# Optimization experiments

Measured on AMD Instinct MI355X. Metric: run time of the kernel, lower is better.

The kernel has to match this reference:

```python
import jax, jax.numpy as jnp
import numpy as np

B, L, D, H, K = 8, 2048, 1024, 4, 4
HD = D // H  # head_dim = 256
EPS_NORM = 1e-12  # F.normalize clamp
RMS_EPS = 1e-05


def setup_inputs() -> dict:
    key = jax.random.key(0)
    ks = jax.random.split(key, 10)
    s = 0.02
    return {
        "x": jax.random.normal(ks[0], (B, L, D), dtype=jnp.float32),
        "Wq": jax.random.normal(ks[1], (D, D), dtype=jnp.float32) * s,
        "Wk": jax.random.normal(ks[2], (D, D), dtype=jnp.float32) * s,
        "Wv": jax.random.normal(ks[3], (D, D), dtype=jnp.float32) * s,
        "cq": jax.random.normal(ks[4], (D, 1, K), dtype=jnp.float32) * 0.2,
        "ck": jax.random.normal(ks[5], (D, 1, K), dtype=jnp.float32) * 0.2,
        "cv": jax.random.normal(ks[6], (D, 1, K), dtype=jnp.float32) * 0.2,
        "Wbeta": jax.random.normal(ks[7], (H, D), dtype=jnp.float32) * s,
        "rms_w": jnp.ones((D,), dtype=jnp.float32),
        "Wout": jax.random.normal(ks[8], (D, D), dtype=jnp.float32) * s,
    }


def _causal_dwconv_silu(y, w):
    # y: [B, L, D], w: [D, 1, K] (torch Conv1d depthwise weight, cross-correlation)
    yt = jnp.transpose(y, (0, 2, 1))  # [B, D, L]
    out = jax.lax.conv_general_dilated(
        yt, w, window_strides=(1,), padding=[(K - 1, 0)],
        dimension_numbers=("NCH", "OIH", "NCH"), feature_group_count=D)
    return jnp.transpose(jax.nn.silu(out), (0, 2, 1))  # [B, L, D]


def _l2norm(x):
    n = jnp.sqrt(jnp.sum(x * x, axis=-1, keepdims=True))
    return x / jnp.maximum(n, EPS_NORM)


def reference(x, Wq, Wk, Wv, cq, ck, cv, Wbeta, rms_w, Wout):
    q = x @ Wq.T
    k = x @ Wk.T
    v = x @ Wv.T
    # depthwise causal conv + silu, then reshape to heads, then silu again (as in source)
    q = jax.nn.silu(_causal_dwconv_silu(q, cq).reshape(B, L, H, HD))
    k = jax.nn.silu(_causal_dwconv_silu(k, ck).reshape(B, L, H, HD))
    v = jax.nn.silu(_causal_dwconv_silu(v, cv).reshape(B, L, H, HD))
    q = _l2norm(q)
    k = _l2norm(k)
    beta = jax.nn.sigmoid(x @ Wbeta.T)  # [B, L, H]

    # time-major for scan: [L, B, H, d]
    kT = jnp.transpose(k, (1, 0, 2, 3))
    qT = jnp.transpose(q, (1, 0, 2, 3))
    vT = jnp.transpose(v, (1, 0, 2, 3))
    bT = jnp.transpose(beta, (1, 0, 2))  # [L, B, H]

    S0 = jnp.zeros((B, H, HD, HD), dtype=x.dtype)

    def step(S, inp):
        k_t, q_t, v_t, b_t = inp
        Sk = jnp.einsum("bhij,bhj->bhi", S, k_t)
        upd = (Sk - v_t)[..., :, None] * k_t[..., None, :]  # outer product [B,H,d,d]
        S = S - b_t[..., None, None] * upd
        o = jnp.einsum("bhij,bhj->bhi", S, q_t)
        return S, o

    S_final, o_all = jax.lax.scan(step, S0, (kT, qT, vT, bT))
    o = o_all[-1].reshape(B, D)  # only last timestep's output is used

    # RMSNorm + output projection
    o = o * jax.lax.rsqrt(jnp.mean(o * o, axis=-1, keepdims=True) + RMS_EPS) * rms_w
    o = o @ Wout.T
    return o, S_final
```

## Files before the change

### kernel.cpp

```cpp
#include <hip/hip_runtime.h>

#define LL 2048
#define BB 8
#define DD 1024
#define HH 4
#define HD 256

#define AS1 __attribute__((address_space(1)))
#define AS3 __attribute__((address_space(3)))

typedef __attribute__((ext_vector_type(8))) short short8;
typedef __attribute__((ext_vector_type(4))) float f32x4;
typedef unsigned short u16;
typedef unsigned int u32;

static __device__ __forceinline__ u16 f2bf(float f) {
    u32 u = __float_as_uint(f);
    return (u16)((u + 0x7fffu + ((u >> 16) & 1u)) >> 16);
}
static __device__ __forceinline__ float bf2f(u16 v) {
    return __uint_as_float(((u32)v) << 16);
}
static __device__ __forceinline__ float silu_f(float x) { return x / (1.0f + __expf(-x)); }
static __device__ __forceinline__ float silu2_fast(float x) {
    float s1 = x * __builtin_amdgcn_rcpf(1.0f + __expf(-x));
    return s1 * __builtin_amdgcn_rcpf(1.0f + __expf(-s1));
}

#define BAR_LGKM() do { \
    asm volatile("s_waitcnt lgkmcnt(0)" ::: "memory"); \
    __builtin_amdgcn_s_barrier(); \
    __builtin_amdgcn_sched_barrier(0); \
} while (0)

static __device__ __forceinline__ void cvt8_body(const float* __restrict__ in,
                                                 u16* __restrict__ out, int blk, int n) {
    int i = (blk * 256 + (int)threadIdx.x) * 8;
    if (i >= n) return;
    float4 a = *(const float4*)(in + i);
    float4 b = *(const float4*)(in + i + 4);
    uint4 pk;
    pk.x = (u32)f2bf(a.x) | ((u32)f2bf(a.y) << 16);
    pk.y = (u32)f2bf(a.z) | ((u32)f2bf(a.w) << 16);
    pk.z = (u32)f2bf(b.x) | ((u32)f2bf(b.y) << 16);
    pk.w = (u32)f2bf(b.z) | ((u32)f2bf(b.w) << 16);
    *(uint4*)(out + i) = pk;
}

__global__ __launch_bounds__(256) void front_kernel(
    const float* __restrict__ x, const float* __restrict__ Wk, const float* __restrict__ Wv,
    const float* __restrict__ Wbeta, const float* __restrict__ Wq,
    u16* __restrict__ XB, u16* __restrict__ WKVB, float* __restrict__ BETA,
    u16* __restrict__ RQ)
{
    const int blk = blockIdx.x;
    const int tid = threadIdx.x;
    if (blk < 8192) {
        cvt8_body(x, XB, blk, 16777216);
    } else if (blk < 8704) {
        cvt8_body(Wk, WKVB, blk - 8192, 1048576);
    } else if (blk < 9216) {
        cvt8_body(Wv, WKVB + 1048576, blk - 8704, 1048576);
    } else if (blk < 13312) {
        const int row = (blk - 9216) * 4 + (tid >> 6);
        const int lane = tid & 63;
        const float* xr = x + (long)row * DD + lane * 16;
        float4 xv[4];
#pragma unroll
        for (int u = 0; u < 4; u++) xv[u] = *(const float4*)(xr + u * 4);
#pragma unroll
        for (int h = 0; h < 4; h++) {
            const float* wr = Wbeta + (long)h * DD + lane * 16;
            float s = 0.f;
#pragma unroll
            for (int u = 0; u < 4; u++) {
                float4 w = *(const float4*)(wr + u * 4);
                s += xv[u].x * w.x + xv[u].y * w.y + xv[u].z * w.z + xv[u].w * w.w;
            }
#pragma unroll
            for (int m = 1; m < 64; m <<= 1) s += __shfl_xor(s, m);
            if (lane == 0) BETA[(long)row * HH + h] = 1.0f / (1.0f + __expf(-s));
        }
    } else {
        const int gid = (blk - 13312) * 4 + (tid >> 6);
        const int lane = tid & 63;
        const int m = gid >> 10;
        const int n = gid & 1023;
        const int b = m >> 2, j = m & 3;
        const int l = LL - 4 + j;
        const float* xr = x + ((long)b * LL + l) * DD + lane * 16;
        const float* wr = Wq + (long)n * DD + lane * 16;
        float s = 0.f;
#pragma unroll
        for (int u = 0; u < 4; u++) {
            float4 a = *(const float4*)(xr + u * 4);
            float4 w = *(const float4*)(wr + u * 4);
            s += a.x * w.x + a.y * w.y + a.z * w.z + a.w * w.w;
        }
#pragma unroll
        for (int mm = 1; mm < 64; mm <<= 1) s += __shfl_xor(s, mm);
        if (lane == 0) RQ[(long)m * DD + n] = f2bf(s);
    }
}

__global__ __launch_bounds__(256, 2) void gemm_bf16(const u16* __restrict__ A,
                                                    const u16* __restrict__ W,
                                                    u16* __restrict__ C, int ldc) {
    __shared__ __align__(16) u16 sm[32768];
    const int tid = threadIdx.x;
    const int w = tid >> 6, lane = tid & 63, g = lane >> 4, c = lane & 15;
    const int m0 = blockIdx.y * 128, n0 = blockIdx.x * 128;
    const int wm = (w >> 1) * 64, wn = (w & 1) * 64;

    f32x4 acc[4][4];
#pragma unroll
    for (int i = 0; i < 4; i++)
#pragma unroll
        for (int j = 0; j < 4; j++) acc[i][j] = (f32x4){0.f, 0.f, 0.f, 0.f};

    const int sr = tid >> 3;
    const int cb = (tid & 7) * 16;

#define GLDSG(gp, lofs) __builtin_amdgcn_global_load_lds((const AS1 void*)(gp), \
        (AS3 void*)((AS3 char*)(char*)sm + (lofs)), 16, 0, 0)

#define GSTAGE(kt, bi)                                                        \
    {                                                                         \
        const char* ab = (const char*)(A + (long)m0 * DD + (kt) * 64);        \
        const char* wb = (const char*)(W + (long)n0 * DD + (kt) * 64);        \
        _Pragma("unroll")                                                     \
        for (int i = 0; i < 4; i++) {                                         \
            int r = i * 32 + sr;                                              \
            int so = r * 2048 + (cb ^ ((r & 7) << 4));                        \
            int dof = (bi) * 32768 + i * 4096 + tid * 16;                     \
            GLDSG(ab + so, dof);                                              \
            GLDSG(wb + so, dof + 16384);                                      \
        }                                                                     \
    }

    GSTAGE(0, 0);
    __syncthreads();

    const int sw = (c & 7) << 4;
    for (int kt = 0; kt < 16; kt++) {
        const int bi = kt & 1;
        if (kt < 15) GSTAGE(kt + 1, bi ^ 1);
        const int ba = bi * 32768;
#pragma unroll
        for (int ks = 0; ks < 2; ks++) {
            short8 av[4], bvv[4];
#pragma unroll
            for (int mt = 0; mt < 4; mt++)
                av[mt] = *(const short8*)((const char*)sm + ba +
                         (wm + 16 * mt + c) * 128 + ((ks * 64 + g * 16) ^ sw));
#pragma unroll
            for (int nt = 0; nt < 4; nt++)
                bvv[nt] = *(const short8*)((const char*)sm + ba + 16384 +
                          (wn + 16 * nt + c) * 128 + ((ks * 64 + g * 16) ^ sw));
#pragma unroll
            for (int mt = 0; mt < 4; mt++)
#pragma unroll
                for (int nt = 0; nt < 4; nt++)
                    acc[mt][nt] = __builtin_amdgcn_mfma_f32_16x16x32_bf16(av[mt], bvv[nt], acc[mt][nt], 0, 0, 0);
        }
        __syncthreads();
    }

#pragma unroll
    for (int mt = 0; mt < 4; mt++)
#pragma unroll
        for (int nt = 0; nt < 4; nt++)
#pragma unroll
            for (int r = 0; r < 4; r++)
                C[(long)(m0 + wm + 16 * mt + 4 * g + r) * ldc + n0 + wn + 16 * nt + c] =
                    f2bf(acc[mt][nt][r]);
#undef GSTAGE
#undef GLDSG
}

__global__ __launch_bounds__(256, 2) void prep_fused(
    const u16* __restrict__ R, const float* __restrict__ ck, const float* __restrict__ cv,
    const float* __restrict__ cq, const u16* __restrict__ RQ, const float* __restrict__ BETA,
    u16* __restrict__ LK_g, u16* __restrict__ BKT_g, u16* __restrict__ LV_g,
    u16* __restrict__ QN)
{
    __shared__ __align__(16) char pm[66560];
    const int blk = blockIdx.x;
    const int tid = threadIdx.x;

    if (blk >= 1024) {
        const int b = blk - 1024;
        const int d = tid * 4;
        float w0[4], w1[4], w2[4], w3[4];
        const float4* cw4 = (const float4*)cq;
        *(float4*)w0 = cw4[d + 0];
        *(float4*)w1 = cw4[d + 1];
        *(float4*)w2 = cw4[d + 2];
        *(float4*)w3 = cw4[d + 3];
        const u16* base = RQ + (long)b * 4 * DD + d;
        float a0 = 0.f, a1 = 0.f, a2 = 0.f, a3 = 0.f;
#pragma unroll
        for (int j = 0; j < 4; j++) {
            uint2 v = *(const uint2*)(base + (long)j * DD);
            a0 += bf2f((u16)(v.x & 0xffff)) * w0[j];
            a1 += bf2f((u16)(v.x >> 16)) * w1[j];
            a2 += bf2f((u16)(v.y & 0xffff)) * w2[j];
            a3 += bf2f((u16)(v.y >> 16)) * w3[j];
        }
        float y0 = silu2_fast(a0);
        float y1 = silu2_fast(a1);
        float y2 = silu2_fast(a2);
        float y3 = silu2_fast(a3);
        float ss = y0 * y0 + y1 * y1 + y2 * y2 + y3 * y3;
#pragma unroll
        for (int m = 1; m < 64; m <<= 1) ss += __shfl_xor(ss, m);
        float sc = 1.0f / fmaxf(sqrtf(ss), 1e-12f);
        y0 *= sc; y1 *= sc; y2 *= sc; y3 *= sc;
        uint2 o;
        o.x = (u32)f2bf(y0) | ((u32)f2bf(y1) << 16);
        o.y = (u32)f2bf(y2) | ((u32)f2bf(y3) << 16);
        *(uint2*)(QN + ((long)b * 4 + 3) * DD + d) = o;
        return;
    }

    const int bh = blk >> 5, q = blk & 31;
    const int b = bh >> 2, h = bh & 3;
    const int w = tid >> 6, lane = tid & 63, g = lane >> 4, c = lane & 15;
    const long cb = (long)(bh * 32 + q);
    u16* WLp = (u16*)(pm + 32768);
    float* bv   = (float*)(pm + 65536);
    float* n2   = (float*)(pm + 65792);
    float* invn = (float*)(pm + 66048);
    float* ncl  = (float*)(pm + 66304);

    if (tid < 64) bv[tid] = BETA[((long)b * LL + 64 * q + tid) * HH + h];
    {
        float4 wt = ((const float4*)ck)[h * HD + tid];
        const u16* rp = R + ((long)b * LL + 64 * q) * 2048 + h * HD + tid;
#pragma unroll
        for (int hh = 0; hh < 2; hh++) {
            u16 arr[35];
            if (q == 0 && hh == 0) {
                arr[0] = 0; arr[1] = 0; arr[2] = 0;
#pragma unroll
                for (int i = 3; i < 35; i++) arr[i] = rp[(long)(i - 3) * 2048];
            } else {
                const u16* rb = rp + (long)(32 * hh - 3) * 2048;
#pragma unroll
                for (int i = 0; i < 35; i++) arr[i] = rb[(long)i * 2048];
            }
            u16 vals[8];
#pragma unroll
            for (int jj = 0; jj < 32; jj++) {
                int t = 32 * hh + jj;
                float y = bf2f(arr[jj]) * wt.x + bf2f(arr[jj + 1]) * wt.y +
                          bf2f(arr[jj + 2]) * wt.z + bf2f(arr[jj + 3]) * wt.w;
                y = silu2_fast(y);
                u16 yb = f2bf(y);
                vals[t & 7] = yb;
                *(u16*)(pm + 32768 + t * 512 + ((((tid >> 3) ^ (t & 7)) << 4) + (tid & 7) * 2)) = yb;
                if ((t & 7) == 7)
                    *(uint4*)(pm + tid * 128 + (((t >> 3) ^ (tid & 7)) << 4)) = *(uint4*)vals;
            }
        }
    }
    BAR_LGKM();

    f32x4 aacc[4];
#pragma unroll
    for (int nt = 0; nt < 4; nt++) aacc[nt] = (f32x4){0.f, 0.f, 0.f, 0.f};
    {
        const int ra = 16 * w + c;
#pragma unroll
        for (int q8 = 0; q8 < 8; q8++) {
            short8 af = *(const short8*)(pm + 32768 + ra * 512 + (((4 * q8 + g) ^ (ra & 7)) << 4));
#pragma unroll
            for (int nt = 0; nt < 4; nt++) {
                const int rb = 16 * nt + c;
                short8 bf = *(const short8*)(pm + 32768 + rb * 512 + (((4 * q8 + g) ^ (rb & 7)) << 4));
                aacc[nt] = __builtin_amdgcn_mfma_f32_16x16x32_bf16(af, bf, aacc[nt], 0, 0, 0);
            }
        }
    }
#pragma unroll
    for (int nt = 0; nt < 4; nt++)
        if (nt == w && (c >> 2) == g) n2[16 * w + c] = aacc[nt][c & 3];
    BAR_LGKM();
    if (tid < 64) {
        float nn = fmaxf(sqrtf(n2[tid]), 1e-12f);
        ncl[tid] = nn;
        invn[tid] = 1.0f / nn;
    }
    BAR_LGKM();
    {
#pragma unroll
        for (int nt = 0; nt < 4; nt++)
#pragma unroll
            for (int r = 0; r < 4; r++) {
                int tt = 16 * w + 4 * g + r, s = 16 * nt + c;
                WLp[tt * 68 + s] = f2bf(aacc[nt][r] * bv[s] * invn[tt] * invn[s]);
            }
        for (int ii = tid; ii < 2048; ii += 256) {
            int dd = ii >> 3, bl = ii & 7;
            u16 vals[8];
            *(uint4*)vals = *(const uint4*)(pm + dd * 128 + bl * 16);
            int t0 = (bl ^ (dd & 7)) << 3;
#pragma unroll
            for (int j = 0; j < 8; j++)
                vals[j] = f2bf(bf2f(vals[j]) * bv[t0 + j] * invn[t0 + j]);
            *(uint4*)((char*)(BKT_g + cb * 16384) + dd * 128 + bl * 16) = *(uint4*)vals;
        }
    }
    BAR_LGKM();

    {
        const int col = 16 * w + c;
        const float sc_col = invn[col];
        float li[16];
#pragma unroll
        for (int u = 0; u < 16; u++) li[u] = (4 * u + g == col) ? 1.0f : 0.0f;
#pragma unroll
        for (int t = 1; t < 64; t++) {
            float acc = 0.f;
#pragma unroll
            for (int u = 0; u <= (t - 1) / 4; u++) {
                int s = 4 * u + g;
                if (s < t) acc += bf2f(WLp[t * 68 + s]) * li[u];
            }
            acc += __shfl_xor(acc, 16);
            acc += __shfl_xor(acc, 32);
            float val = ((t == col) ? 1.0f : 0.0f) - acc;
            if ((t & 3) == g) li[t >> 2] = val;
        }
#pragma unroll
        for (int u = 0; u < 16; u++) {
            int s = 4 * u + g;
            *(u16*)(pm + 41472 + s * 128 + ((((col >> 3) ^ (s & 7)) << 4) + (col & 7) * 2)) =
                f2bf(li[u] * sc_col);
        }
    }
    BAR_LGKM();

    {
        f32x4 lk[4][4];
#pragma unroll
        for (int i = 0; i < 4; i++)
#pragma unroll
            for (int j = 0; j < 4; j++) lk[i][j] = (f32x4){0.f, 0.f, 0.f, 0.f};
#pragma unroll
        for (int qs = 0; qs < 2; qs++) {
            short8 aL[4], bK[4];
#pragma unroll
            for (int mt = 0; mt < 4; mt++)
                aL[mt] = *(const short8*)(pm + 41472 + (16 * mt + c) * 128 +
                                          (((qs * 4 + g) ^ (c & 7)) << 4));
#pragma unroll
            for (int dn = 0; dn < 4; dn++)
                bK[dn] = *(const short8*)(pm + (64 * w + 16 * dn + c) * 128 +
                                          (((qs * 4 + g) ^ (c & 7)) << 4));
#pragma unroll
            for (int mt = 0; mt < 4; mt++)
#pragma unroll
                for (int dn = 0; dn < 4; dn++)
                    lk[mt][dn] = __builtin_amdgcn_mfma_f32_16x16x32_bf16(aL[mt], bK[dn], lk[mt][dn], 0, 0, 0);
        }
        char* lkg = (char*)(LK_g + cb * 16384);
#pragma unroll
        for (int mt = 0; mt < 4; mt++)
#pragma unroll
            for (int dn = 0; dn < 4; dn++)
#pragma unroll
                for (int r = 0; r < 4; r++) {
                    int t = 16 * mt + 4 * g + r;
                    int d = 64 * w + 16 * dn + c;
                    *(u16*)(lkg + t * 512 + ((((d >> 3) ^ (t & 7)) << 4) + (d & 7) * 2)) =
                        f2bf(-lk[mt][dn][r]);
                }
    }
    BAR_LGKM();

    {
        float4 wt = ((const float4*)cv)[h * HD + tid];
        const u16* rp = R + ((long)b * LL + 64 * q) * 2048 + 1024 + h * HD + tid;
#pragma unroll
        for (int hh = 0; hh < 2; hh++) {
            u16 arr[35];
            if (q == 0 && hh == 0) {
                arr[0] = 0; arr[1] = 0; arr[2] = 0;
#pragma unroll
                for (int i = 3; i < 35; i++) arr[i] = rp[(long)(i - 3) * 2048];
            } else {
                const u16* rb = rp + (long)(32 * hh - 3) * 2048;
#pragma unroll
                for (int i = 0; i < 35; i++) arr[i] = rb[(long)i * 2048];
            }
            u16 vals[8];
#pragma unroll
            for (int jj = 0; jj < 32; jj++) {
                int t = 32 * hh + jj;
                float y = bf2f(arr[jj]) * wt.x + bf2f(arr[jj + 1]) * wt.y +
                          bf2f(arr[jj + 2]) * wt.z + bf2f(arr[jj + 3]) * wt.w;
                y = silu2_fast(y) * ncl[t];
                vals[t & 7] = f2bf(y);
                if ((t & 7) == 7)
                    *(uint4*)(pm + tid * 128 + (((t >> 3) ^ (tid & 7)) << 4)) = *(uint4*)vals;
            }
        }
    }
    BAR_LGKM();

    {
        f32x4 lv[4][4];
#pragma unroll
        for (int i = 0; i < 4; i++)
#pragma unroll
            for (int j = 0; j < 4; j++) lv[i][j] = (f32x4){0.f, 0.f, 0.f, 0.f};
#pragma unroll
        for (int qs = 0; qs < 2; qs++) {
            short8 aL[4], bV[4];
#pragma unroll
            for (int mt = 0; mt < 4; mt++)
                aL[mt] = *(const short8*)(pm + 41472 + (16 * mt + c) * 128 +
                                          (((qs * 4 + g) ^ (c & 7)) << 4));
#pragma unroll
            for (int dn = 0; dn < 4; dn++)
                bV[dn] = *(const short8*)(pm + (64 * w + 16 * dn + c) * 128 +
                                          (((qs * 4 + g) ^ (c & 7)) << 4));
#pragma unroll
            for (int mt = 0; mt < 4; mt++)
#pragma unroll
                for (int dn = 0; dn < 4; dn++)
                    lv[mt][dn] = __builtin_amdgcn_mfma_f32_16x16x32_bf16(aL[mt], bV[dn], lv[mt][dn], 0, 0, 0);
        }
        u32* lvg = (u32*)LV_g + cb * 8192;
#pragma unroll
        for (int mt = 0; mt < 4; mt++)
#pragma unroll
            for (int dn = 0; dn < 4; dn++) {
                int iblk = 2 * w + (dn >> 1);
                int it = dn & 1;
                int base = iblk * 1024 + 64 * (2 * mt + it) + 16 * g + c;
                lvg[base]       = (u32)f2bf(lv[mt][dn][0]) | ((u32)f2bf(lv[mt][dn][1]) << 16);
                lvg[base + 512] = (u32)f2bf(lv[mt][dn][2]) | ((u32)f2bf(lv[mt][dn][3]) << 16);
            }
    }
}

__global__ __launch_bounds__(512, 1) void scan_chunked(
    const u16* __restrict__ LK_g, const u16* __restrict__ BKT_g,
    const u16* __restrict__ LV_g, const u16* __restrict__ QN,
    float* __restrict__ out, float* __restrict__ ORAW)
{
    __shared__ __align__(16) char smem[159744];
    const int blk = blockIdx.x;
    const int bh = blk & 31, iblk = blk >> 5;
    const int b = bh >> 2, h = bh & 3;
    const int row0 = iblk * 32;
    const int tid = threadIdx.x;
    const int w = tid >> 6, lane = tid & 63, g = lane >> 4, c = lane & 15;
    const int mt = w >> 1, it = w & 1;
    const int sw = (c & 7) << 4;

#define GLDS16(gp, lofs) __builtin_amdgcn_global_load_lds((const AS1 void*)(gp), \
        (AS3 void*)((AS3 char*)smem + (lofs)), 16, 0, 0)
#define GLDS4(gp, lofs) __builtin_amdgcn_global_load_lds((const AS1 void*)(gp), \
        (AS3 void*)((AS3 char*)smem + (lofs)), 4, 0, 0)
#define STAGE_LK(qq, bi) { const char* gp = (const char*)(LK_g + (long)(bh * 32 + (qq)) * 16384); \
    _Pragma("unroll") for (int i_ = 0; i_ < 4; i_++) GLDS16(gp + i_ * 8192 + tid * 16, (bi) * 32768 + i_ * 8192 + tid * 16); }
#define STAGE_BKT(qq, bi) { const char* gp = (const char*)(BKT_g + (long)(bh * 32 + (qq)) * 16384); \
    _Pragma("unroll") for (int i_ = 0; i_ < 4; i_++) GLDS16(gp + i_ * 8192 + tid * 16, 65536 + (bi) * 32768 + i_ * 8192 + tid * 16); }
#define STAGE_LV(qq, bi) { const char* gp = (const char*)LV_g + (long)(bh * 32 + (qq)) * 32768 + iblk * 4096; \
    GLDS4(gp + tid * 4, 131072 + (bi) * 4096 + tid * 4); \
    GLDS4(gp + 2048 + tid * 4, 131072 + (bi) * 4096 + 2048 + tid * 4); }

    f32x4 S[2][2];
#pragma unroll
    for (int si = 0; si < 2; si++)
#pragma unroll
        for (int sj = 0; sj < 2; sj++) S[si][sj] = (f32x4){0.f, 0.f, 0.f, 0.f};

    STAGE_LK(0, 0); STAGE_BKT(0, 0); STAGE_LV(0, 0);

    for (int q = 0; q < 32; ++q) {
        const int cur = q & 1;
        if (q < 31) {
            STAGE_LK(q + 1, cur ^ 1); STAGE_BKT(q + 1, cur ^ 1); STAGE_LV(q + 1, cur ^ 1);
            asm volatile("s_waitcnt vmcnt(10)" ::: "memory");
        } else {
            asm volatile("s_waitcnt vmcnt(0)" ::: "memory");
        }
        __builtin_amdgcn_s_barrier();
        __builtin_amdgcn_sched_barrier(0);

        const char* lkb = smem + cur * 32768;
        const char* bkb = smem + 65536 + cur * 32768;
        const char* lvb = smem + 131072 + cur * 4096;

        u32 l0 = *(const u32*)(lvb + tid * 4);
        u32 l1 = *(const u32*)(lvb + 2048 + tid * 4);
        f32x4 w0, w1;
        w0[0] = bf2f((u16)(l0 & 0xffff)); w0[1] = bf2f((u16)(l0 >> 16));
        w0[2] = bf2f((u16)(l1 & 0xffff)); w0[3] = bf2f((u16)(l1 >> 16));
        w1 = (f32x4){0.f, 0.f, 0.f, 0.f};
        if (q > 0) {
            const int arow = (16 * mt + c) * 512;
            const int brow = (16 * it + c) * 512;
            __builtin_amdgcn_s_setprio(1);
#pragma unroll
            for (int q8 = 0; q8 < 8; q8++) {
                short8 av = *(const short8*)(lkb + arow + (((q8 * 4 + g) << 4) ^ sw));
                short8 bv8 = *(const short8*)(smem + 143360 + brow + (((q8 * 4 + g) << 4) ^ sw));
                if (q8 & 1) w1 = __builtin_amdgcn_mfma_f32_16x16x32_bf16(av, bv8, w1, 0, 0, 0);
                else        w0 = __builtin_amdgcn_mfma_f32_16x16x32_bf16(av, bv8, w0, 0, 0, 0);
            }
            __builtin_amdgcn_s_setprio(0);
#pragma unroll
            for (int r = 0; r < 4; r++) w0[r] += w1[r];
        }

        {
            char* ub = smem + 139264 + (16 * it + c) * 128;
#pragma unroll
            for (int r = 0; r < 4; r++) {
                int t = 16 * mt + 4 * g + r;
                *(u16*)(ub + ((((t >> 3) << 4) ^ sw) + (t & 7) * 2)) = f2bf(w0[r]);
            }
        }
        asm volatile("s_waitcnt lgkmcnt(0)" ::: "memory");
        __builtin_amdgcn_s_barrier();
        __builtin_amdgcn_sched_barrier(0);

        __builtin_amdgcn_s_setprio(1);
#pragma unroll
        for (int Qp = 0; Qp < 2; Qp++) {
            const int tof = ((Qp * 4 + g) << 4) ^ sw;
            short8 a0 = *(const short8*)(smem + 139264 + c * 128 + tof);
            short8 a1 = *(const short8*)(smem + 139264 + (16 + c) * 128 + tof);
            short8 b0 = *(const short8*)(bkb + (32 * w + c) * 128 + tof);
            short8 b1 = *(const short8*)(bkb + (32 * w + 16 + c) * 128 + tof);
            S[0][0] = __builtin_amdgcn_mfma_f32_16x16x32_bf16(a0, b0, S[0][0], 0, 0, 0);
            S[0][1] = __builtin_amdgcn_mfma_f32_16x16x32_bf16(a0, b1, S[0][1], 0, 0, 0);
            S[1][0] = __builtin_amdgcn_mfma_f32_16x16x32_bf16(a1, b0, S[1][0], 0, 0, 0);
            S[1][1] = __builtin_amdgcn_mfma_f32_16x16x32_bf16(a1, b1, S[1][1], 0, 0, 0);
        }
        __builtin_amdgcn_s_setprio(0);

        if (q < 31) {
#pragma unroll
            for (int si = 0; si < 2; si++)
#pragma unroll
                for (int sj = 0; sj < 2; sj++)
#pragma unroll
                    for (int r = 0; r < 4; r++) {
                        int i = 16 * si + 4 * g + r;
                        *(u16*)(smem + 143360 + i * 512 +
                                ((((4 * w + 2 * sj + (c >> 3)) << 4) ^ ((i & 7) << 4)) + (c & 7) * 2)) =
                            f2bf(S[si][sj][r]);
                    }
        }
        asm volatile("s_waitcnt lgkmcnt(0)" ::: "memory");
        __builtin_amdgcn_s_barrier();
        __builtin_amdgcn_sched_barrier(0);
    }

    float op[2][4];
#pragma unroll
    for (int si = 0; si < 2; si++)
#pragma unroll
        for (int r = 0; r < 4; r++) op[si][r] = 0.f;
#pragma unroll
    for (int sj = 0; sj < 2; sj++) {
        const float qv = bf2f(QN[((long)b * 4 + 3) * DD + h * HD + 32 * w + 16 * sj + c]);
#pragma unroll
        for (int si = 0; si < 2; si++)
#pragma unroll
            for (int r = 0; r < 4; r++) op[si][r] += S[si][sj][r] * qv;
    }
#pragma unroll
    for (int si = 0; si < 2; si++)
#pragma unroll
        for (int r = 0; r < 4; r++) {
            float v = op[si][r];
            v += __shfl_xor(v, 1); v += __shfl_xor(v, 2);
            v += __shfl_xor(v, 4); v += __shfl_xor(v, 8);
            op[si][r] = v;
        }
    float* red = (float*)smem;
    if (c == 0) {
#pragma unroll
        for (int si = 0; si < 2; si++)
#pragma unroll
            for (int r = 0; r < 4; r++) red[w * 32 + 16 * si + 4 * g + r] = op[si][r];
    }
    __syncthreads();
    if (tid < 32) {
        float o = 0.f;
#pragma unroll
        for (int ww = 0; ww < 8; ww++) o += red[ww * 32 + tid];
        ORAW[(long)b * DD + h * HD + row0 + tid] = o;
    }
#pragma unroll
    for (int si = 0; si < 2; si++)
#pragma unroll
        for (int sj = 0; sj < 2; sj++)
#pragma unroll
            for (int r = 0; r < 4; r++)
                out[8192 + ((long)(bh * 256 + row0 + 16 * si + 4 * g + r)) * 256
                    + 32 * w + 16 * sj + c] = S[si][sj][r];
#undef GLDS16
#undef GLDS4
#undef STAGE_LK
#undef STAGE_BKT
#undef STAGE_LV
}

__global__ __launch_bounds__(256) void tail_kernel(const float* __restrict__ ORAW,
                                                   const float* __restrict__ rms_w,
                                                   const float* __restrict__ Wout,
                                                   float* __restrict__ out) {
    const int b = blockIdx.x >> 8;
    const int n = (blockIdx.x & 255) * 4 + (threadIdx.x >> 6);
    const int lane = threadIdx.x & 63;
    const int t = threadIdx.x;

    float4 v = *(const float4*)(ORAW + (long)b * DD + t * 4);
    float ss = v.x * v.x + v.y * v.y + v.z * v.z + v.w * v.w;
#pragma unroll
    for (int m = 1; m < 64; m <<= 1) ss += __shfl_xor(ss, m);
    __shared__ float wsum[4];
    if ((t & 63) == 0) wsum[t >> 6] = ss;
    __syncthreads();
    float tot = wsum[0] + wsum[1] + wsum[2] + wsum[3];
    float sc = rsqrtf(tot / (float)DD + 1e-5f);

    const float* orow = ORAW + (long)b * DD + lane * 16;
    const float* grow = rms_w + lane * 16;
    const float* wrow = Wout + (long)n * DD + lane * 16;
    float s = 0.f;
#pragma unroll
    for (int u = 0; u < 4; u++) {
        float4 a = *(const float4*)(orow + u * 4);
        float4 gw = *(const float4*)(grow + u * 4);
        float4 ww = *(const float4*)(wrow + u * 4);
        s += a.x * sc * gw.x * ww.x + a.y * sc * gw.y * ww.y +
             a.z * sc * gw.z * ww.z + a.w * sc * gw.w * ww.w;
    }
#pragma unroll
    for (int m = 1; m < 64; m <<= 1) s += __shfl_xor(s, m);
    if (lane == 0) out[(long)b * DD + n] = s;
}

extern "C" void kernel_launch(void* const* d_in, const int* in_sizes, int n_in,
                              void* d_out, int out_size, void* d_ws, size_t ws_size,
                              hipStream_t stream) {
    const float* x     = (const float*)d_in[0];
    const float* Wq    = (const float*)d_in[1];
    const float* Wk    = (const float*)d_in[2];
    const float* Wv    = (const float*)d_in[3];
    const float* cq    = (const float*)d_in[4];
    const float* ck    = (const float*)d_in[5];
    const float* cv    = (const float*)d_in[6];
    const float* Wbeta = (const float*)d_in[7];
    const float* rms_w = (const float*)d_in[8];
    const float* Wout  = (const float*)d_in[9];
    float* out = (float*)d_out;

    char* ws = (char*)d_ws;
    u16* XB     = (u16*)(ws + 0);
    u16* BKT_g  = (u16*)(ws + 0);
    u16* WKVB   = (u16*)(ws + 33554432);
    u16* R      = (u16*)(ws + 37748736);
    u16* LK_g   = (u16*)(ws + 104857600);
    u16* LV_g   = (u16*)(ws + 138412032);
    float* BETA = (float*)(ws + 171966464);
    u16* RQ     = (u16*)(ws + 172228608);
    u16* QN     = (u16*)(ws + 172294144);
    float* ORAW = (float*)(ws + 172359680);

    front_kernel<<<21504, 256, 0, stream>>>(x, Wk, Wv, Wbeta, Wq, XB, WKVB, BETA, RQ);
    gemm_bf16<<<dim3(16, 128), 256, 0, stream>>>(XB, WKVB, R, 2048);
    prep_fused<<<1032, 256, 0, stream>>>(R, ck, cv, cq, RQ, BETA, LK_g, BKT_g, LV_g, QN);
    scan_chunked<<<256, 512, 0, stream>>>(LK_g, BKT_g, LV_g, QN, out, ORAW);
    tail_kernel<<<2048, 256, 0, stream>>>(ORAW, rms_w, Wout, out);
}
```

Before: 262.7 us.

## Double scan block to 1024 threads, splitting K-reduction and S columns across waves

The chunked scan kernel now runs 16 waves per block instead of 8. The W computation's K-dimension is split across wave pairs, with partial results written to two LDS buffers (WA/WB) that are summed inside the S-update MFMAs. Each wave now owns a 16-column slice of S instead of 32. The LV chunk is loaded straight into registers one chunk ahead rather than staged through LDS. The goal is more latency hiding and shorter per-wave serial work on the sequential scan. The cost is extra MFMAs to combine the partials, more LDS reads, and a wider final reduction.

```diff
diff --git a/kernel.cpp b/kernel.cpp
--- a/kernel.cpp
+++ b/kernel.cpp
@@ -446,46 +446,49 @@
     }
 }
 
-__global__ __launch_bounds__(512, 1) void scan_chunked(
+__global__ __launch_bounds__(1024, 1) void scan_chunked(
     const u16* __restrict__ LK_g, const u16* __restrict__ BKT_g,
     const u16* __restrict__ LV_g, const u16* __restrict__ QN,
     float* __restrict__ out, float* __restrict__ ORAW)
 {
-    __shared__ __align__(16) char smem[159744];
+    __shared__ __align__(16) char smem[155648];
     const int blk = blockIdx.x;
     const int bh = blk & 31, iblk = blk >> 5;
     const int b = bh >> 2, h = bh & 3;
     const int row0 = iblk * 32;
     const int tid = threadIdx.x;
     const int w = tid >> 6, lane = tid & 63, g = lane >> 4, c = lane & 15;
-    const int mt = w >> 1, it = w & 1;
+    const int mt = w >> 2, it = (w >> 1) & 1, jh = w & 1;
     const int sw = (c & 7) << 4;
 
 #define GLDS16(gp, lofs) __builtin_amdgcn_global_load_lds((const AS1 void*)(gp), \
         (AS3 void*)((AS3 char*)smem + (lofs)), 16, 0, 0)
-#define GLDS4(gp, lofs) __builtin_amdgcn_global_load_lds((const AS1 void*)(gp), \
-        (AS3 void*)((AS3 char*)smem + (lofs)), 4, 0, 0)
 #define STAGE_LK(qq, bi) { const char* gp = (const char*)(LK_g + (long)(bh * 32 + (qq)) * 16384); \
-    _Pragma("unroll") for (int i_ = 0; i_ < 4; i_++) GLDS16(gp + i_ * 8192 + tid * 16, (bi) * 32768 + i_ * 8192 + tid * 16); }
+    _Pragma("unroll") for (int i_ = 0; i_ < 2; i_++) GLDS16(gp + i_ * 16384 + tid * 16, (bi) * 32768 + i_ * 16384 + tid * 16); }
 #define STAGE_BKT(qq, bi) { const char* gp = (const char*)(BKT_g + (long)(bh * 32 + (qq)) * 16384); \
-    _Pragma("unroll") for (int i_ = 0; i_ < 4; i_++) GLDS16(gp + i_ * 8192 + tid * 16, 65536 + (bi) * 32768 + i_ * 8192 + tid * 16); }
-#define STAGE_LV(qq, bi) { const char* gp = (const char*)LV_g + (long)(bh * 32 + (qq)) * 32768 + iblk * 4096; \
-    GLDS4(gp + tid * 4, 131072 + (bi) * 4096 + tid * 4); \
-    GLDS4(gp + 2048 + tid * 4, 131072 + (bi) * 4096 + 2048 + tid * 4); }
-
-    f32x4 S[2][2];
-#pragma unroll
-    for (int si = 0; si < 2; si++)
-#pragma unroll
-        for (int sj = 0; sj < 2; sj++) S[si][sj] = (f32x4){0.f, 0.f, 0.f, 0.f};
-
-    STAGE_LK(0, 0); STAGE_BKT(0, 0); STAGE_LV(0, 0);
+    _Pragma("unroll") for (int i_ = 0; i_ < 2; i_++) GLDS16(gp + i_ * 16384 + tid * 16, 65536 + (bi) * 32768 + i_ * 16384 + tid * 16); }
+
+    const int lvidx = 64 * (w >> 1) + lane;
+#define LV_PTR(qq) ((const u32*)((const char*)LV_g + (long)(bh * 32 + (qq)) * 32768 + iblk * 4096) + lvidx)
+
+    char* const WA = smem + 131072;
+    char* const WB = smem + 135168;
+    char* const TS = smem + 139264;
+
+    f32x4 S[2];
+    S[0] = (f32x4){0.f, 0.f, 0.f, 0.f};
+    S[1] = (f32x4){0.f, 0.f, 0.f, 0.f};
+
+    u32 lc0 = LV_PTR(0)[0], lc1 = LV_PTR(0)[512];
+    STAGE_LK(0, 0); STAGE_BKT(0, 0);
+    u32 ln0 = 0, ln1 = 0;
 
     for (int q = 0; q < 32; ++q) {
         const int cur = q & 1;
         if (q < 31) {
-            STAGE_LK(q + 1, cur ^ 1); STAGE_BKT(q + 1, cur ^ 1); STAGE_LV(q + 1, cur ^ 1);
-            asm volatile("s_waitcnt vmcnt(10)" ::: "memory");
+            ln0 = LV_PTR(q + 1)[0]; ln1 = LV_PTR(q + 1)[512];
+            STAGE_LK(q + 1, cur ^ 1); STAGE_BKT(q + 1, cur ^ 1);
+            asm volatile("s_waitcnt vmcnt(6)" ::: "memory");
         } else {
             asm volatile("s_waitcnt vmcnt(0)" ::: "memory");
         }
@@ -494,23 +497,25 @@
 
         const char* lkb = smem + cur * 32768;
         const char* bkb = smem + 65536 + cur * 32768;
-        const char* lvb = smem + 131072 + cur * 4096;
-
-        u32 l0 = *(const u32*)(lvb + tid * 4);
-        u32 l1 = *(const u32*)(lvb + 2048 + tid * 4);
+
         f32x4 w0, w1;
-        w0[0] = bf2f((u16)(l0 & 0xffff)); w0[1] = bf2f((u16)(l0 >> 16));
-        w0[2] = bf2f((u16)(l1 & 0xffff)); w0[3] = bf2f((u16)(l1 >> 16));
+        if (jh == 0) {
+            w0[0] = bf2f((u16)(lc0 & 0xffff)); w0[1] = bf2f((u16)(lc0 >> 16));
+            w0[2] = bf2f((u16)(lc1 & 0xffff)); w0[3] = bf2f((u16)(lc1 >> 16));
+        } else {
+            w0 = (f32x4){0.f, 0.f, 0.f, 0.f};
+        }
         w1 = (f32x4){0.f, 0.f, 0.f, 0.f};
         if (q > 0) {
             const int arow = (16 * mt + c) * 512;
             const int brow = (16 * it + c) * 512;
             __builtin_amdgcn_s_setprio(1);
 #pragma unroll
-            for (int q8 = 0; q8 < 8; q8++) {
+            for (int k8 = 0; k8 < 4; k8++) {
+                const int q8 = jh * 4 + k8;
                 short8 av = *(const short8*)(lkb + arow + (((q8 * 4 + g) << 4) ^ sw));
-                short8 bv8 = *(const short8*)(smem + 143360 + brow + (((q8 * 4 + g) << 4) ^ sw));
-                if (q8 & 1) w1 = __builtin_amdgcn_mfma_f32_16x16x32_bf16(av, bv8, w1, 0, 0, 0);
+                short8 bv8 = *(const short8*)(TS + brow + (((q8 * 4 + g) << 4) ^ sw));
+                if (k8 & 1) w1 = __builtin_amdgcn_mfma_f32_16x16x32_bf16(av, bv8, w1, 0, 0, 0);
                 else        w0 = __builtin_amdgcn_mfma_f32_16x16x32_bf16(av, bv8, w0, 0, 0, 0);
             }
             __builtin_amdgcn_s_setprio(0);
@@ -519,7 +524,7 @@
         }
 
         {
-            char* ub = smem + 139264 + (16 * it + c) * 128;
+            char* ub = (jh ? WB : WA) + (16 * it + c) * 128;
 #pragma unroll
             for (int r = 0; r < 4; r++) {
                 int t = 16 * mt + 4 * g + r;
@@ -534,14 +539,15 @@
 #pragma unroll
         for (int Qp = 0; Qp < 2; Qp++) {
             const int tof = ((Qp * 4 + g) << 4) ^ sw;
-            short8 a0 = *(const short8*)(smem + 139264 + c * 128 + tof);
-            short8 a1 = *(const short8*)(smem + 139264 + (16 + c) * 128 + tof);
-            short8 b0 = *(const short8*)(bkb + (32 * w + c) * 128 + tof);
-            short8 b1 = *(const short8*)(bkb + (32 * w + 16 + c) * 128 + tof);
-            S[0][0] = __builtin_amdgcn_mfma_f32_16x16x32_bf16(a0, b0, S[0][0], 0, 0, 0);
-            S[0][1] = __builtin_amdgcn_mfma_f32_16x16x32_bf16(a0, b1, S[0][1], 0, 0, 0);
-            S[1][0] = __builtin_amdgcn_mfma_f32_16x16x32_bf16(a1, b0, S[1][0], 0, 0, 0);
-            S[1][1] = __builtin_amdgcn_mfma_f32_16x16x32_bf16(a1, b1, S[1][1], 0, 0, 0);
+            short8 b0  = *(const short8*)(bkb + (16 * w + c) * 128 + tof);
+            short8 a0a = *(const short8*)(WA + c * 128 + tof);
+            short8 a1a = *(const short8*)(WA + (16 + c) * 128 + tof);
+            short8 a0b = *(const short8*)(WB + c * 128 + tof);
+            short8 a1b = *(const short8*)(WB + (16 + c) * 128 + tof);
+            S[0] = __builtin_amdgcn_mfma_f32_16x16x32_bf16(a0a, b0, S[0], 0, 0, 0);
+            S[1] = __builtin_amdgcn_mfma_f32_16x16x32_bf16(a1a, b0, S[1], 0, 0, 0);
+            S[0] = __builtin_amdgcn_mfma_f32_16x16x32_bf16(a0b, b0, S[0], 0, 0, 0);
+            S[1] = __builtin_amdgcn_mfma_f32_16x16x32_bf16(a1b, b0, S[1], 0, 0, 0);
         }
         __builtin_amdgcn_s_setprio(0);
 
@@ -549,18 +555,17 @@
 #pragma unroll
             for (int si = 0; si < 2; si++)
 #pragma unroll
-                for (int sj = 0; sj < 2; sj++)
-#pragma unroll
-                    for (int r = 0; r < 4; r++) {
-                        int i = 16 * si + 4 * g + r;
-                        *(u16*)(smem + 143360 + i * 512 +
-                                ((((4 * w + 2 * sj + (c >> 3)) << 4) ^ ((i & 7) << 4)) + (c & 7) * 2)) =
-                            f2bf(S[si][sj][r]);
-                    }
+                for (int r = 0; r < 4; r++) {
+                    int i = 16 * si + 4 * g + r;
+                    *(u16*)(TS + i * 512 +
+                            ((((2 * w + (c >> 3)) << 4) ^ ((i & 7) << 4)) + (c & 7) * 2)) =
+                        f2bf(S[si][r]);
+                }
         }
         asm volatile("s_waitcnt lgkmcnt(0)" ::: "memory");
         __builtin_amdgcn_s_barrier();
         __builtin_amdgcn_sched_barrier(0);
+        lc0 = ln0; lc1 = ln1;
     }
 
     float op[2][4];
@@ -568,13 +573,12 @@
     for (int si = 0; si < 2; si++)
 #pragma unroll
         for (int r = 0; r < 4; r++) op[si][r] = 0.f;
-#pragma unroll
-    for (int sj = 0; sj < 2; sj++) {
-        const float qv = bf2f(QN[((long)b * 4 + 3) * DD + h * HD + 32 * w + 16 * sj + c]);
+    {
+        const float qv = bf2f(QN[((long)b * 4 + 3) * DD + h * HD + 16 * w + c]);
 #pragma unroll
         for (int si = 0; si < 2; si++)
 #pragma unroll
-            for (int r = 0; r < 4; r++) op[si][r] += S[si][sj][r] * qv;
+            for (int r = 0; r < 4; r++) op[si][r] += S[si][r] * qv;
     }
 #pragma unroll
     for (int si = 0; si < 2; si++)
@@ -596,22 +600,19 @@
     if (tid < 32) {
         float o = 0.f;
 #pragma unroll
-        for (int ww = 0; ww < 8; ww++) o += red[ww * 32 + tid];
+        for (int ww = 0; ww < 16; ww++) o += red[ww * 32 + tid];
         ORAW[(long)b * DD + h * HD + row0 + tid] = o;
     }
 #pragma unroll
     for (int si = 0; si < 2; si++)
 #pragma unroll
-        for (int sj = 0; sj < 2; sj++)
-#pragma unroll
-            for (int r = 0; r < 4; r++)
-                out[8192 + ((long)(bh * 256 + row0 + 16 * si + 4 * g + r)) * 256
-                    + 32 * w + 16 * sj + c] = S[si][sj][r];
+        for (int r = 0; r < 4; r++)
+            out[8192 + ((long)(bh * 256 + row0 + 16 * si + 4 * g + r)) * 256
+                + 16 * w + c] = S[si][r];
 #undef GLDS16
-#undef GLDS4
 #undef STAGE_LK
 #undef STAGE_BKT
-#undef STAGE_LV
+#undef LV_PTR
 }
 
 __global__ __launch_bounds__(256) void tail_kernel(const float* __restrict__ ORAW,
@@ -680,6 +681,6 @@
     front_kernel<<<21504, 256, 0, stream>>>(x, Wk, Wv, Wbeta, Wq, XB, WKVB, BETA, RQ);
     gemm_bf16<<<dim3(16, 128), 256, 0, stream>>>(XB, WKVB, R, 2048);
     prep_fused<<<1032, 256, 0, stream>>>(R, ck, cv, cq, RQ, BETA, LK_g, BKT_g, LV_g, QN);
-    scan_chunked<<<256, 512, 0, stream>>>(LK_g, BKT_g, LV_g, QN, out, ORAW);
+    scan_chunked<<<256, 1024, 0, stream>>>(LK_g, BKT_g, LV_g, QN, out, ORAW);
     tail_kernel<<<2048, 256, 0, stream>>>(ORAW, rms_w, Wout, out);
 }
```

After: 271.4 us. +3.3%, slower.

## Replace KV projection GEMM with 256x256-tile eight-phase pipelined bf16 kernel

Applied to the files above, without the earlier changes.

Swaps the 128x128-tile, 256-thread double-buffered GEMM for a 256x256-tile, 512-thread kernel using 128 KB of LDS. The k-loop is split into eight phases that interleave global-to-LDS loads with quarter-tile MFMA blocks, with explicit barriers, vmcnt waits and s_setprio. The aim is more reuse of each staged tile and better overlap of memory traffic with matrix math. In exchange, occupancy drops to one block per CU, the grid has only 512 blocks, and the hand-written waitcnt/barrier choreography is fragile.

```diff
diff --git a/kernel.cpp b/kernel.cpp
--- a/kernel.cpp
+++ b/kernel.cpp
@@ -103,79 +103,103 @@
     }
 }
 
-__global__ __launch_bounds__(256, 2) void gemm_bf16(const u16* __restrict__ A,
-                                                    const u16* __restrict__ W,
-                                                    u16* __restrict__ C, int ldc) {
-    __shared__ __align__(16) u16 sm[32768];
+__global__ __launch_bounds__(512, 1) void gemm_8ph(const u16* __restrict__ A,
+                                                   const u16* __restrict__ W,
+                                                   u16* __restrict__ C) {
+    __shared__ __align__(16) char sm_[131072];
     const int tid = threadIdx.x;
     const int w = tid >> 6, lane = tid & 63, g = lane >> 4, c = lane & 15;
-    const int m0 = blockIdx.y * 128, n0 = blockIdx.x * 128;
-    const int wm = (w >> 1) * 64, wn = (w & 1) * 64;
-
-    f32x4 acc[4][4];
-#pragma unroll
-    for (int i = 0; i < 4; i++)
+    const int wm_ = w >> 2, wn_ = w & 3;
+    const int m0 = blockIdx.y * 256, n0 = blockIdx.x * 256;
+    const int sr = tid >> 3, cb = (tid & 7) * 16;
+    const int ssw = (sr & 7) << 4;
+    const int sw = (c & 7) << 4;
+
+    f32x4 acc[8][4];
+#pragma unroll
+    for (int i = 0; i < 8; i++)
 #pragma unroll
         for (int j = 0; j < 4; j++) acc[i][j] = (f32x4){0.f, 0.f, 0.f, 0.f};
-
-    const int sr = tid >> 3;
-    const int cb = (tid & 7) * 16;
-
-#define GLDSG(gp, lofs) __builtin_amdgcn_global_load_lds((const AS1 void*)(gp), \
-        (AS3 void*)((AS3 char*)(char*)sm + (lofs)), 16, 0, 0)
-
-#define GSTAGE(kt, bi)                                                        \
-    {                                                                         \
-        const char* ab = (const char*)(A + (long)m0 * DD + (kt) * 64);        \
-        const char* wb = (const char*)(W + (long)n0 * DD + (kt) * 64);        \
-        _Pragma("unroll")                                                     \
-        for (int i = 0; i < 4; i++) {                                         \
-            int r = i * 32 + sr;                                              \
-            int so = r * 2048 + (cb ^ ((r & 7) << 4));                        \
-            int dof = (bi) * 32768 + i * 4096 + tid * 16;                     \
-            GLDSG(ab + so, dof);                                              \
-            GLDSG(wb + so, dof + 16384);                                      \
-        }                                                                     \
-    }
-
-    GSTAGE(0, 0);
-    __syncthreads();
-
-    const int sw = (c & 7) << 4;
-    for (int kt = 0; kt < 16; kt++) {
-        const int bi = kt & 1;
-        if (kt < 15) GSTAGE(kt + 1, bi ^ 1);
-        const int ba = bi * 32768;
-#pragma unroll
-        for (int ks = 0; ks < 2; ks++) {
-            short8 av[4], bvv[4];
-#pragma unroll
-            for (int mt = 0; mt < 4; mt++)
-                av[mt] = *(const short8*)((const char*)sm + ba +
-                         (wm + 16 * mt + c) * 128 + ((ks * 64 + g * 16) ^ sw));
-#pragma unroll
-            for (int nt = 0; nt < 4; nt++)
-                bvv[nt] = *(const short8*)((const char*)sm + ba + 16384 +
-                          (wn + 16 * nt + c) * 128 + ((ks * 64 + g * 16) ^ sw));
-#pragma unroll
-            for (int mt = 0; mt < 4; mt++)
-#pragma unroll
-                for (int nt = 0; nt < 4; nt++)
-                    acc[mt][nt] = __builtin_amdgcn_mfma_f32_16x16x32_bf16(av[mt], bvv[nt], acc[mt][nt], 0, 0, 0);
-        }
-        __syncthreads();
-    }
-
-#pragma unroll
-    for (int mt = 0; mt < 4; mt++)
+    short8 afr[4][2];
+    short8 bfr[2][2];
+
+#define GL8(gp, lofs) __builtin_amdgcn_global_load_lds((const AS1 void*)(gp), \
+        (AS3 void*)((AS3 char*)sm_ + (lofs)), 16, 0, 0)
+#define ST_A(kt, half, PB) { \
+    const char* gp_ = (const char*)A + ((long)(m0 + (half)*128 + sr) * 1024 + (kt) * 64) * 2 + (cb ^ ssw); \
+    GL8(gp_, (PB) + (half)*16384 + tid*16); GL8(gp_ + 131072, (PB) + (half)*16384 + 8192 + tid*16); }
+#define ST_B(kt, half, PB) { \
+    const char* gp_ = (const char*)W + ((long)(n0 + (half)*128 + sr) * 1024 + (kt) * 64) * 2 + (cb ^ ssw); \
+    GL8(gp_, 65536 + (PB) + (half)*16384 + tid*16); GL8(gp_ + 131072, 65536 + (PB) + (half)*16384 + 8192 + tid*16); }
+#define LOADA(qm, PB) { \
+    const char* ab_ = sm_ + (PB) + wm_ * 16384 + ((qm) * 64 + c) * 128; \
+    _Pragma("unroll") for (int mt = 0; mt < 4; mt++) \
+        _Pragma("unroll") for (int ks = 0; ks < 2; ks++) \
+            afr[mt][ks] = *(const short8*)(ab_ + mt * 2048 + ((ks * 64 + g * 16) ^ sw)); }
+#define LOADB(qn, PB) { \
+    const char* bb_ = sm_ + 65536 + (PB) + (wn_ >> 1) * 16384 + ((wn_ & 1) * 64 + (qn) * 32 + c) * 128; \
+    _Pragma("unroll") for (int nt = 0; nt < 2; nt++) \
+        _Pragma("unroll") for (int ks = 0; ks < 2; ks++) \
+            bfr[nt][ks] = *(const short8*)(bb_ + nt * 2048 + ((ks * 64 + g * 16) ^ sw)); }
+#define MFMAQ(qm, qn) { \
+    __builtin_amdgcn_s_barrier(); \
+    __builtin_amdgcn_s_setprio(1); \
+    _Pragma("unroll") for (int mt = 0; mt < 4; mt++) \
+        _Pragma("unroll") for (int nt = 0; nt < 2; nt++) \
+            _Pragma("unroll") for (int ks = 0; ks < 2; ks++) \
+                acc[(qm)*4+mt][(qn)*2+nt] = __builtin_amdgcn_mfma_f32_16x16x32_bf16( \
+                    afr[mt][ks], bfr[nt][ks], acc[(qm)*4+mt][(qn)*2+nt], 0, 0, 0); \
+    __builtin_amdgcn_s_setprio(0); }
+#define ENDB() { __builtin_amdgcn_s_barrier(); __builtin_amdgcn_sched_barrier(0); }
+
+    ST_A(0, 0, 0) ST_A(0, 1, 0) ST_B(0, 0, 0) ST_B(0, 1, 0) ST_A(1, 0, 32768)
+    asm volatile("s_waitcnt vmcnt(2)" ::: "memory");
+    __builtin_amdgcn_s_barrier();
+    __builtin_amdgcn_sched_barrier(0);
+
+    for (int u = 0; u < 8; ++u) {
+        const int t1k = 2 * u + 1, nk = 2 * u + 2, nk1 = 2 * u + 3;
+        const bool more = (u < 7);
+        LOADA(0, 0) LOADB(0, 0) ST_A(t1k, 1, 32768) MFMAQ(0, 0) ENDB()
+        LOADB(1, 0) ST_B(t1k, 0, 32768) MFMAQ(0, 1) ENDB()
+        LOADA(1, 0) LOADB(0, 0) ST_B(t1k, 1, 32768) MFMAQ(1, 0) ENDB()
+        LOADB(1, 0)
+        if (more) ST_A(nk, 0, 0)
+        MFMAQ(1, 1)
+        if (more) { asm volatile("s_waitcnt vmcnt(2)" ::: "memory"); }
+        else      { asm volatile("s_waitcnt vmcnt(0)" ::: "memory"); }
+        ENDB()
+        LOADA(0, 32768) LOADB(0, 32768)
+        if (more) ST_B(nk, 0, 0)
+        MFMAQ(0, 0) ENDB()
+        LOADB(1, 32768)
+        if (more) ST_A(nk, 1, 0)
+        MFMAQ(0, 1) ENDB()
+        LOADA(1, 32768) LOADB(0, 32768)
+        if (more) ST_B(nk, 1, 0)
+        MFMAQ(1, 0) ENDB()
+        LOADB(1, 32768)
+        if (more) ST_A(nk1, 0, 32768)
+        MFMAQ(1, 1)
+        if (more) { asm volatile("s_waitcnt vmcnt(2)" ::: "memory"); }
+        ENDB()
+    }
+
+#pragma unroll
+    for (int mt = 0; mt < 8; mt++)
 #pragma unroll
         for (int nt = 0; nt < 4; nt++)
 #pragma unroll
             for (int r = 0; r < 4; r++)
-                C[(long)(m0 + wm + 16 * mt + 4 * g + r) * ldc + n0 + wn + 16 * nt + c] =
-                    f2bf(acc[mt][nt][r]);
-#undef GSTAGE
-#undef GLDSG
+                C[(long)(m0 + wm_ * 128 + mt * 16 + 4 * g + r) * 2048 +
+                  n0 + wn_ * 64 + nt * 16 + c] = f2bf(acc[mt][nt][r]);
+#undef GL8
+#undef ST_A
+#undef ST_B
+#undef LOADA
+#undef LOADB
+#undef MFMAQ
+#undef ENDB
 }
 
 __global__ __launch_bounds__(256, 2) void prep_fused(
@@ -678,7 +702,7 @@
     float* ORAW = (float*)(ws + 172359680);
 
     front_kernel<<<21504, 256, 0, stream>>>(x, Wk, Wv, Wbeta, Wq, XB, WKVB, BETA, RQ);
-    gemm_bf16<<<dim3(16, 128), 256, 0, stream>>>(XB, WKVB, R, 2048);
+    gemm_8ph<<<dim3(8, 64), 512, 0, stream>>>(XB, WKVB, R);
     prep_fused<<<1032, 256, 0, stream>>>(R, ck, cv, cq, RQ, BETA, LK_g, BKT_g, LV_g, QN);
     scan_chunked<<<256, 512, 0, stream>>>(LK_g, BKT_g, LV_g, QN, out, ORAW);
     tail_kernel<<<2048, 256, 0, stream>>>(ORAW, rms_w, Wout, out);
```

Result: faster. 249.6 us (-5.0%).
